# Kernel tuning notes

Hardware: AMD Instinct MI355X
Metric: run time of the kernel (lower is better)

Reference implementation:

```python
import jax, jax.numpy as jnp
import numpy as np

N = 8192
IN_F = 512
OUT_F = 64
ALPHA = 0.2   # LeakyReLU negative slope
STDV = 0.2
NEG_INF = -9e15


def setup_inputs() -> dict:
    key = jax.random.key(0)
    k1, k2, k3, k4 = jax.random.split(key, 4)
    x = jax.random.normal(k1, (N, IN_F), dtype=jnp.float32)
    adj = jax.random.randint(k2, (N, N), 0, 2, dtype=jnp.int32)
    W = jax.random.normal(k3, (IN_F, OUT_F), dtype=jnp.float32) * STDV
    a = jax.random.normal(k4, (2 * OUT_F, 1), dtype=jnp.float32) * STDV
    return {"x": x, "adj": adj, "W": W, "a": a}


def reference(x, adj, W, a):
    # Wh: [N, F']
    Wh = x @ W
    # attention logits: e[i,j] = leakyrelu(Wh[i]@a1 + Wh[j]@a2)
    Wh1 = Wh @ a[:OUT_F, :]   # [N, 1]
    Wh2 = Wh @ a[OUT_F:, :]   # [N, 1]
    e = Wh1 + Wh2.T           # [N, N] via broadcast
    e = jnp.where(e >= 0, e, ALPHA * e)  # LeakyReLU
    # mask by adjacency, row softmax
    masked = jnp.where(adj > 0, e, jnp.float32(NEG_INF))
    attention = jax.nn.softmax(masked, axis=1)
    # dropout rate is 0.0 in this config -> identity
    h_prime = attention @ Wh  # [N, F']
    out = jnp.where(h_prime > 0, h_prime, jnp.expm1(h_prime))  # ELU
    return out, attention
```

## Files before the change

kernel.cpp:

```cpp
#include <hip/hip_runtime.h>
#include <cmath>

#define Nn    8192
#define INF_  512
#define OUTF  64

typedef __attribute__((ext_vector_type(4))) int   i4;
typedef __attribute__((ext_vector_type(4))) float f4v;
typedef __attribute__((ext_vector_type(8))) short s8;
typedef __attribute__((ext_vector_type(4))) float f32x4;
typedef unsigned long long u64;

__device__ __forceinline__ float lrelu(float v) { return fmaxf(v, 0.2f * v); }

__device__ __forceinline__ unsigned int f2bf(float f) {
    unsigned int u = __float_as_uint(f);
    u = (u + 0x7FFFu + ((u >> 16) & 1u)) >> 16;
    return u;
}

__global__ __launch_bounds__(1024, 8) void k1_wh(
    const float* __restrict__ x, const float* __restrict__ W,
    const float* __restrict__ a, unsigned short* __restrict__ WhT,
    float* __restrict__ Wh1, float* __restrict__ Wh2)
{
    __shared__ float part[3][16][64];
    __shared__ unsigned short stage[64][16];
    const int t    = threadIdx.x;
    const int s    = t >> 8;
    const int r    = (t >> 4) & 15;
    const int cg   = (t & 15) << 2;
    const int row0 = blockIdx.x * 16;
    const int row  = row0 + r;
    const float* __restrict__ xr = x + (size_t)row * INF_ + s * 128;
    const float* __restrict__ Wp = W + (size_t)s * 128 * OUTF;

    float4 acc = make_float4(0.f, 0.f, 0.f, 0.f);
    for (int k = 0; k < 128; k += 4) {
        const float4 xv = *(const float4*)(xr + k);
        const float* wp = Wp + (size_t)k * OUTF + cg;
        const float4 w0 = *(const float4*)(wp);
        const float4 w1 = *(const float4*)(wp + OUTF);
        const float4 w2 = *(const float4*)(wp + 2 * OUTF);
        const float4 w3 = *(const float4*)(wp + 3 * OUTF);
        acc.x += xv.x * w0.x + xv.y * w1.x + xv.z * w2.x + xv.w * w3.x;
        acc.y += xv.x * w0.y + xv.y * w1.y + xv.z * w2.y + xv.w * w3.y;
        acc.z += xv.x * w0.z + xv.y * w1.z + xv.z * w2.z + xv.w * w3.z;
        acc.w += xv.x * w0.w + xv.y * w1.w + xv.z * w2.w + xv.w * w3.w;
    }
    if (s > 0) *(float4*)&part[s - 1][r][cg] = acc;
    __syncthreads();
    if (s == 0) {
        const float4 pa = *(const float4*)&part[0][r][cg];
        const float4 pb = *(const float4*)&part[1][r][cg];
        const float4 pc = *(const float4*)&part[2][r][cg];
        acc.x += pa.x + pb.x + pc.x;
        acc.y += pa.y + pb.y + pc.y;
        acc.z += pa.z + pb.z + pc.z;
        acc.w += pa.w + pb.w + pc.w;
        stage[cg + 0][r] = (unsigned short)f2bf(acc.x);
        stage[cg + 1][r] = (unsigned short)f2bf(acc.y);
        stage[cg + 2][r] = (unsigned short)f2bf(acc.z);
        stage[cg + 3][r] = (unsigned short)f2bf(acc.w);

        float p1 = acc.x * a[cg]        + acc.y * a[cg + 1]
                 + acc.z * a[cg + 2]    + acc.w * a[cg + 3];
        float p2 = acc.x * a[OUTF + cg]     + acc.y * a[OUTF + cg + 1]
                 + acc.z * a[OUTF + cg + 2] + acc.w * a[OUTF + cg + 3];
        #pragma unroll
        for (int off = 8; off; off >>= 1) {
            p1 += __shfl_xor(p1, off);
            p2 += __shfl_xor(p2, off);
        }
        if ((t & 15) == 0) { Wh1[row] = p1; Wh2[row] = p2; }
    }
    __syncthreads();
    if (t < 256) {
        const int col = t >> 2;
        const int q   = t & 3;
        const u64 v = *(const u64*)&stage[col][q * 4];
        *(u64*)(WhT + (size_t)col * Nn + row0 + q * 4) = v;
    }
}

__global__ __launch_bounds__(1024, 8) void k2_fused(
    const int* __restrict__ adj, const unsigned short* __restrict__ WhT,
    const float* __restrict__ Wh1, const float* __restrict__ Wh2,
    float* __restrict__ outp, float* __restrict__ att)
{
    __shared__ alignas(16) unsigned short att_t[2][16 * 256];
    __shared__ float red[3][4][16][16];

    const int t    = threadIdx.x;
    const int lane = t & 63;
    const int w    = t >> 6;
    const int row0 = blockIdx.x * 16;
    const int row  = row0 + w;
    const int* __restrict__ adjrow = adj + (size_t)row * Nn;
    const float h1 = Wh1[row];

    u64 mk0 = 0, mk1 = 0;
    float S = 0.f;
    #pragma unroll 4
    for (int i = 0; i < 16; ++i) {
        const i4  av = __builtin_nontemporal_load((const i4*)(adjrow + 256 * i) + lane);
        const f4v w4 = *((const f4v*)(Wh2 + 256 * i) + lane);
        const int nib = (av.x != 0 ? 1 : 0) | (av.y != 0 ? 2 : 0)
                      | (av.z != 0 ? 4 : 0) | (av.w != 0 ? 8 : 0);
        S += (nib & 1) ? __expf(lrelu(h1 + w4.x)) : 0.f;
        S += (nib & 2) ? __expf(lrelu(h1 + w4.y)) : 0.f;
        S += (nib & 4) ? __expf(lrelu(h1 + w4.z)) : 0.f;
        S += (nib & 8) ? __expf(lrelu(h1 + w4.w)) : 0.f;
        mk0 |= (u64)nib << (i * 4);
    }
    #pragma unroll 4
    for (int i = 16; i < 32; ++i) {
        const i4  av = __builtin_nontemporal_load((const i4*)(adjrow + 256 * i) + lane);
        const f4v w4 = *((const f4v*)(Wh2 + 256 * i) + lane);
        const int nib = (av.x != 0 ? 1 : 0) | (av.y != 0 ? 2 : 0)
                      | (av.z != 0 ? 4 : 0) | (av.w != 0 ? 8 : 0);
        S += (nib & 1) ? __expf(lrelu(h1 + w4.x)) : 0.f;
        S += (nib & 2) ? __expf(lrelu(h1 + w4.y)) : 0.f;
        S += (nib & 4) ? __expf(lrelu(h1 + w4.z)) : 0.f;
        S += (nib & 8) ? __expf(lrelu(h1 + w4.w)) : 0.f;
        mk1 |= (u64)nib << ((i - 16) * 4);
    }
    #pragma unroll
    for (int off = 32; off; off >>= 1) S += __shfl_xor(S, off);
    const float is = 1.0f / S;

    const int ct = w & 3;
    const int kq = w >> 2;
    f32x4 acc = {0.f, 0.f, 0.f, 0.f};

    auto produce_lds = [&](int c, int bf) {
        const int jb = c * 256;
        const f4v w2 = *((const f4v*)(Wh2 + jb) + lane);
        const int nib = (int)(((c & 16) ? mk1 : mk0) >> ((c & 15) * 4)) & 15;
        const float v0 = (nib & 1) ? __expf(lrelu(h1 + w2.x)) * is : 0.f;
        const float v1 = (nib & 2) ? __expf(lrelu(h1 + w2.y)) * is : 0.f;
        const float v2 = (nib & 4) ? __expf(lrelu(h1 + w2.z)) * is : 0.f;
        const float v3 = (nib & 8) ? __expf(lrelu(h1 + w2.w)) * is : 0.f;
        const u64 pk = (u64)(f2bf(v0) | (f2bf(v1) << 16))
                     | ((u64)(f2bf(v2) | (f2bf(v3) << 16)) << 32);
        int byte = w * 512 + lane * 8;  byte ^= (w & 7) << 4;
        *(u64*)((char*)att_t[bf] + byte) = pk;
    };

    const int ar = lane & 15;
    const int ag = lane >> 4;
    auto bload = [&](int c, int ss) -> s8 {
        const int ks = kq * 2 + ss;
        return *(const s8*)(WhT + (size_t)(ct * 16 + ar) * Nn
                            + c * 256 + ks * 32 + ag * 8);
    };
    auto amfma = [&](int c, int bf, s8 b0, s8 b1) {
        #pragma unroll
        for (int ss = 0; ss < 2; ++ss) {
            const int ks = kq * 2 + ss;
            int byte = ar * 512 + ks * 64 + ag * 16;
            byte ^= (ar & 7) << 4;
            const s8 af = *(const s8*)((char*)att_t[bf] + byte);
            acc = __builtin_amdgcn_mfma_f32_16x16x32_bf16(af, ss ? b1 : b0, acc, 0, 0, 0);
        }
    };

    s8 b0 = bload(0, 0), b1 = bload(0, 1);
    produce_lds(0, 0);
    asm volatile("s_waitcnt lgkmcnt(0)" ::: "memory");
    __builtin_amdgcn_s_barrier();
    for (int c = 0; c < Nn / 256 - 1; ++c) {
        const s8 nb0 = bload(c + 1, 0);
        const s8 nb1 = bload(c + 1, 1);
        produce_lds(c + 1, (c + 1) & 1);
        amfma(c, c & 1, b0, b1);
        asm volatile("s_waitcnt lgkmcnt(0)" ::: "memory");
        __builtin_amdgcn_s_barrier();
        b0 = nb0; b1 = nb1;
    }
    amfma(Nn / 256 - 1, (Nn / 256 - 1) & 1, b0, b1);

    __syncthreads();
    if (kq > 0) {
        #pragma unroll
        for (int q = 0; q < 4; ++q) red[kq - 1][ct][ag * 4 + q][ar] = acc[q];
    }
    __syncthreads();
    if (kq == 0) {
        #pragma unroll
        for (int q = 0; q < 4; ++q) {
            const int r = ag * 4 + q;
            float v = acc[q] + red[0][ct][r][ar] + red[1][ct][r][ar] + red[2][ct][r][ar];
            v = v > 0.f ? v : expm1f(v);
            outp[(size_t)(row0 + r) * OUTF + ct * 16 + ar] = v;
        }
    }

    float* __restrict__ arow_out = att + (size_t)row * Nn;
    for (int c = 0; c < 32; ++c) {
        const int jb = c * 256;
        const f4v w2 = *((const f4v*)(Wh2 + jb) + lane);
        const int nib = (int)(((c & 16) ? mk1 : mk0) >> ((c & 15) * 4)) & 15;
        f4v st;
        st.x = (nib & 1) ? __expf(lrelu(h1 + w2.x)) * is : 0.f;
        st.y = (nib & 2) ? __expf(lrelu(h1 + w2.y)) * is : 0.f;
        st.z = (nib & 4) ? __expf(lrelu(h1 + w2.z)) * is : 0.f;
        st.w = (nib & 8) ? __expf(lrelu(h1 + w2.w)) * is : 0.f;
        __builtin_nontemporal_store(st, (f4v*)(arow_out + jb) + lane);
    }
}

extern "C" void kernel_launch(void* const* d_in, const int* in_sizes, int n_in,
                              void* d_out, int out_size, void* d_ws, size_t ws_size,
                              hipStream_t stream)
{
    const float* x   = (const float*)d_in[0];
    const int*   adj = (const int*)d_in[1];
    const float* W   = (const float*)d_in[2];
    const float* a   = (const float*)d_in[3];

    float* outp = (float*)d_out;
    float* att  = outp + (size_t)Nn * OUTF;

    float* Wh1 = (float*)d_ws;
    float* Wh2 = Wh1 + Nn;
    unsigned short* WhT = (unsigned short*)(Wh2 + Nn);

    hipLaunchKernelGGL(k1_wh,    dim3(Nn / 16), dim3(1024), 0, stream,
                       x, W, a, WhT, Wh1, Wh2);
    hipLaunchKernelGGL(k2_fused, dim3(Nn / 16), dim3(1024), 0, stream,
                       adj, WhT, Wh1, Wh2, outp, att);
}
```

Baseline: 186.0 us.

## Fuse softmax denominator pass into MFMA loop with deferred normalization

Removes the separate first pass over the adjacency row that computed the softmax denominator and mask bits. The unnormalized exp values now feed the bf16 MFMA aggregation directly while the sum and mask are accumulated in the same loop, and the output is scaled by 1/S afterwards through a small shared array. This saves one full sweep of exp evaluations and lets adjacency loads be prefetched two chunks ahead, at the cost of rounding unnormalized values to bf16. Launch bounds are also relaxed from 8 to 4 waves per SIMD, which allows more registers per thread.

```diff
diff --git a/kernel.cpp b/kernel.cpp
--- a/kernel.cpp
+++ b/kernel.cpp
@@ -19,7 +19,7 @@
     return u;
 }
 
-__global__ __launch_bounds__(1024, 8) void k1_wh(
+__global__ __launch_bounds__(1024, 4) void k1_wh(
     const float* __restrict__ x, const float* __restrict__ W,
     const float* __restrict__ a, unsigned short* __restrict__ WhT,
     float* __restrict__ Wh1, float* __restrict__ Wh2)
@@ -83,13 +83,14 @@
     }
 }
 
-__global__ __launch_bounds__(1024, 8) void k2_fused(
+__global__ __launch_bounds__(1024, 4) void k2_fused(
     const int* __restrict__ adj, const unsigned short* __restrict__ WhT,
     const float* __restrict__ Wh1, const float* __restrict__ Wh2,
     float* __restrict__ outp, float* __restrict__ att)
 {
     __shared__ alignas(16) unsigned short att_t[2][16 * 256];
     __shared__ float red[3][4][16][16];
+    __shared__ float sm_is[16];
 
     const int t    = threadIdx.x;
     const int lane = t & 63;
@@ -99,62 +100,38 @@
     const int* __restrict__ adjrow = adj + (size_t)row * Nn;
     const float h1 = Wh1[row];
 
+    const int ct = w & 3;
+    const int kq = w >> 2;
+    const int ar = lane & 15;
+    const int ag = lane >> 4;
+
     u64 mk0 = 0, mk1 = 0;
     float S = 0.f;
-    #pragma unroll 4
-    for (int i = 0; i < 16; ++i) {
-        const i4  av = __builtin_nontemporal_load((const i4*)(adjrow + 256 * i) + lane);
-        const f4v w4 = *((const f4v*)(Wh2 + 256 * i) + lane);
+    f32x4 acc = {0.f, 0.f, 0.f, 0.f};
+
+    auto produce = [&](int c, int bf, i4 av) {
+        const f4v w2 = *((const f4v*)(Wh2 + c * 256) + lane);
         const int nib = (av.x != 0 ? 1 : 0) | (av.y != 0 ? 2 : 0)
                       | (av.z != 0 ? 4 : 0) | (av.w != 0 ? 8 : 0);
-        S += (nib & 1) ? __expf(lrelu(h1 + w4.x)) : 0.f;
-        S += (nib & 2) ? __expf(lrelu(h1 + w4.y)) : 0.f;
-        S += (nib & 4) ? __expf(lrelu(h1 + w4.z)) : 0.f;
-        S += (nib & 8) ? __expf(lrelu(h1 + w4.w)) : 0.f;
-        mk0 |= (u64)nib << (i * 4);
-    }
-    #pragma unroll 4
-    for (int i = 16; i < 32; ++i) {
-        const i4  av = __builtin_nontemporal_load((const i4*)(adjrow + 256 * i) + lane);
-        const f4v w4 = *((const f4v*)(Wh2 + 256 * i) + lane);
-        const int nib = (av.x != 0 ? 1 : 0) | (av.y != 0 ? 2 : 0)
-                      | (av.z != 0 ? 4 : 0) | (av.w != 0 ? 8 : 0);
-        S += (nib & 1) ? __expf(lrelu(h1 + w4.x)) : 0.f;
-        S += (nib & 2) ? __expf(lrelu(h1 + w4.y)) : 0.f;
-        S += (nib & 4) ? __expf(lrelu(h1 + w4.z)) : 0.f;
-        S += (nib & 8) ? __expf(lrelu(h1 + w4.w)) : 0.f;
-        mk1 |= (u64)nib << ((i - 16) * 4);
-    }
-    #pragma unroll
-    for (int off = 32; off; off >>= 1) S += __shfl_xor(S, off);
-    const float is = 1.0f / S;
-
-    const int ct = w & 3;
-    const int kq = w >> 2;
-    f32x4 acc = {0.f, 0.f, 0.f, 0.f};
-
-    auto produce_lds = [&](int c, int bf) {
-        const int jb = c * 256;
-        const f4v w2 = *((const f4v*)(Wh2 + jb) + lane);
-        const int nib = (int)(((c & 16) ? mk1 : mk0) >> ((c & 15) * 4)) & 15;
-        const float v0 = (nib & 1) ? __expf(lrelu(h1 + w2.x)) * is : 0.f;
-        const float v1 = (nib & 2) ? __expf(lrelu(h1 + w2.y)) * is : 0.f;
-        const float v2 = (nib & 4) ? __expf(lrelu(h1 + w2.z)) * is : 0.f;
-        const float v3 = (nib & 8) ? __expf(lrelu(h1 + w2.w)) * is : 0.f;
-        const u64 pk = (u64)(f2bf(v0) | (f2bf(v1) << 16))
-                     | ((u64)(f2bf(v2) | (f2bf(v3) << 16)) << 32);
+        if (c < 16) mk0 |= (u64)nib << (c * 4);
+        else        mk1 |= (u64)nib << ((c - 16) * 4);
+        const float p0 = (nib & 1) ? __expf(lrelu(h1 + w2.x)) : 0.f;
+        const float p1 = (nib & 2) ? __expf(lrelu(h1 + w2.y)) : 0.f;
+        const float p2 = (nib & 4) ? __expf(lrelu(h1 + w2.z)) : 0.f;
+        const float p3 = (nib & 8) ? __expf(lrelu(h1 + w2.w)) : 0.f;
+        S += (p0 + p1) + (p2 + p3);
+        const u64 pk = (u64)(f2bf(p0) | (f2bf(p1) << 16))
+                     | ((u64)(f2bf(p2) | (f2bf(p3) << 16)) << 32);
         int byte = w * 512 + lane * 8;  byte ^= (w & 7) << 4;
         *(u64*)((char*)att_t[bf] + byte) = pk;
     };
 
-    const int ar = lane & 15;
-    const int ag = lane >> 4;
     auto bload = [&](int c, int ss) -> s8 {
         const int ks = kq * 2 + ss;
         return *(const s8*)(WhT + (size_t)(ct * 16 + ar) * Nn
                             + c * 256 + ks * 32 + ag * 8);
     };
-    auto amfma = [&](int c, int bf, s8 b0, s8 b1) {
+    auto amfma = [&](int bf, s8 b0, s8 b1) {
         #pragma unroll
         for (int ss = 0; ss < 2; ++ss) {
             const int ks = kq * 2 + ss;
@@ -165,20 +142,33 @@
         }
     };
 
+    i4 av1;
+    {
+        const i4 av0 = __builtin_nontemporal_load((const i4*)(adjrow) + lane);
+        av1 = __builtin_nontemporal_load((const i4*)(adjrow + 256) + lane);
+        produce(0, 0, av0);
+    }
     s8 b0 = bload(0, 0), b1 = bload(0, 1);
-    produce_lds(0, 0);
     asm volatile("s_waitcnt lgkmcnt(0)" ::: "memory");
     __builtin_amdgcn_s_barrier();
-    for (int c = 0; c < Nn / 256 - 1; ++c) {
+    for (int c = 0; c < 31; ++c) {
         const s8 nb0 = bload(c + 1, 0);
         const s8 nb1 = bload(c + 1, 1);
-        produce_lds(c + 1, (c + 1) & 1);
-        amfma(c, c & 1, b0, b1);
+        i4 av2 = {0, 0, 0, 0};
+        if (c + 2 < 32)
+            av2 = __builtin_nontemporal_load((const i4*)(adjrow + 256 * (c + 2)) + lane);
+        produce(c + 1, (c + 1) & 1, av1);
+        amfma(c & 1, b0, b1);
         asm volatile("s_waitcnt lgkmcnt(0)" ::: "memory");
         __builtin_amdgcn_s_barrier();
-        b0 = nb0; b1 = nb1;
-    }
-    amfma(Nn / 256 - 1, (Nn / 256 - 1) & 1, b0, b1);
+        av1 = av2; b0 = nb0; b1 = nb1;
+    }
+    amfma(31 & 1, b0, b1);
+
+    #pragma unroll
+    for (int off = 32; off; off >>= 1) S += __shfl_xor(S, off);
+    const float is = 1.0f / S;
+    if (lane == 0) sm_is[w] = is;
 
     __syncthreads();
     if (kq > 0) {
@@ -191,6 +181,7 @@
         for (int q = 0; q < 4; ++q) {
             const int r = ag * 4 + q;
             float v = acc[q] + red[0][ct][r][ar] + red[1][ct][r][ar] + red[2][ct][r][ar];
+            v *= sm_is[r];
             v = v > 0.f ? v : expm1f(v);
             outp[(size_t)(row0 + r) * OUTF + ct * 16 + ar] = v;
         }
@@ -198,15 +189,14 @@
 
     float* __restrict__ arow_out = att + (size_t)row * Nn;
     for (int c = 0; c < 32; ++c) {
-        const int jb = c * 256;
-        const f4v w2 = *((const f4v*)(Wh2 + jb) + lane);
+        const f4v w2 = *((const f4v*)(Wh2 + c * 256) + lane);
         const int nib = (int)(((c & 16) ? mk1 : mk0) >> ((c & 15) * 4)) & 15;
         f4v st;
         st.x = (nib & 1) ? __expf(lrelu(h1 + w2.x)) * is : 0.f;
         st.y = (nib & 2) ? __expf(lrelu(h1 + w2.y)) * is : 0.f;
         st.z = (nib & 4) ? __expf(lrelu(h1 + w2.z)) * is : 0.f;
         st.w = (nib & 8) ? __expf(lrelu(h1 + w2.w)) * is : 0.f;
-        __builtin_nontemporal_store(st, (f4v*)(arow_out + jb) + lane);
+        __builtin_nontemporal_store(st, (f4v*)(arow_out + c * 256) + lane);
     }
 }
 
```

New measurement: 191.8 us. 3.2% more time.
